# Kernel tuning notes

Measured on AMD Instinct MI355X. Metric: run time of the kernel, lower is better.

Reference implementation:

```python
import jax, jax.numpy as jnp
import numpy as np
from functools import partial

FACTOR = 5
N_HEADS = 16


def setup_inputs() -> dict:
    key = jax.random.key(0)
    ks = jax.random.split(key, 8)
    B, L, D = 4, 4096, 1024
    scale = 0.02
    return {
        "q": jax.random.normal(ks[0], (B, L, D), jnp.float32),
        "k": jax.random.normal(ks[1], (B, L, D), jnp.float32),
        "v": jax.random.normal(ks[2], (B, L, D), jnp.float32),
        "Wq": jax.random.normal(ks[3], (D, D), jnp.float32) * scale,
        "bq": jnp.zeros((D,), jnp.float32),
        "Wk": jax.random.normal(ks[4], (D, D), jnp.float32) * scale,
        "bk": jnp.zeros((D,), jnp.float32),
        "Wv": jax.random.normal(ks[5], (D, D), jnp.float32) * scale,
        "bv": jnp.zeros((D,), jnp.float32),
        "Wo": jax.random.normal(ks[6], (D, D), jnp.float32) * scale,
        "bo": jnp.zeros((D,), jnp.float32),
    }


def _time_delay_agg(values, corr):
    # values, corr: (B, H, L, C).  Faithful to the repo: the double mean
    # over dim=1 reduces head then LENGTH, leaving (B, C); top-k indices
    # therefore live in [0, C) and are reused as time delays.
    B, H, L, C = values.shape
    top_k = int(FACTOR * np.log(L + 1)) if L > 1 else 1
    top_k = max(1, min(top_k, L))
    mean_value = corr.mean(axis=1).mean(axis=1)          # (B, C)
    mean_across_batch = mean_value.mean(axis=0)          # (C,)
    actual_k = min(top_k, C)
    _, indices = jax.lax.top_k(mean_across_batch, actual_k)  # (k,)
    selected = mean_value[:, indices]                    # (B, k)
    weights = jax.nn.softmax(selected, axis=-1)          # (B, k)
    t = jnp.arange(L)

    def body(acc, inp):
        d, w = inp                                       # scalar delay, (B,) weight
        idx = (t + d) % L                                # circular shift == roll of doubled tensor
        acc = acc + values[:, :, idx, :] * w[:, None, None, None]
        return acc, None

    agg, _ = jax.lax.scan(body, jnp.zeros_like(values), (indices, weights.T))
    return agg


def reference(q, k, v, Wq, bq, Wk, bk, Wv, bv, Wo, bo):
    B, L, D = q.shape
    H = N_HEADS
    dk = D // H

    def proj(x, W, b):
        y = x @ W.T + b
        return y.reshape(B, L, H, dk).transpose(0, 2, 1, 3)  # (B,H,L,dk)

    Q = proj(q, Wq, bq).astype(jnp.float32)
    K = proj(k, Wk, bk).astype(jnp.float32)
    V = proj(v, Wv, bv).astype(jnp.float32)

    Qf = jnp.fft.rfft(Q, axis=2)
    Kf = jnp.fft.rfft(K, axis=2)
    R = jnp.fft.irfft(Qf * jnp.conj(Kf), n=L, axis=2)    # (B,H,L,dk) autocorrelation

    V_agg = _time_delay_agg(V, R)                        # (B,H,L,dk)
    V_agg = V_agg.transpose(0, 2, 1, 3).reshape(B, L, D)
    return V_agg @ Wo.T + bo
```

## Files before the change

### kernel.cpp

```cpp
#include <hip/hip_runtime.h>
#include <hip/hip_bf16.h>

#define Bn 4
#define Ln 4096
#define Dn 1024
#define Hn 16
#define KSEL 41
#define NT8 16

typedef __attribute__((ext_vector_type(8))) _Float16 f16x8;
typedef __attribute__((ext_vector_type(4))) float f32x4;

__device__ __forceinline__ unsigned short f2h(float f) {
    union { _Float16 h; unsigned short u; } c;
    c.h = (_Float16)f;
    return c.u;
}

__device__ __forceinline__ void gl2lds16(const unsigned short* g, unsigned short* l) {
    __builtin_amdgcn_global_load_lds(
        (const __attribute__((address_space(1))) unsigned int*)(uintptr_t)g,
        (__attribute__((address_space(3))) unsigned int*)(uintptr_t)l,
        16, 0, 0);
}
__device__ __forceinline__ void gl2lds16f(const float* g, float* l) {
    __builtin_amdgcn_global_load_lds(
        (const __attribute__((address_space(1))) unsigned int*)(uintptr_t)g,
        (__attribute__((address_space(3))) unsigned int*)(uintptr_t)l,
        16, 0, 0);
}

__global__ __launch_bounds__(256) void colsum_part(const float* __restrict__ q,
                                                   const float* __restrict__ k,
                                                   float* __restrict__ part) {
    int tb = blockIdx.y; int tensor = tb >> 2, b = tb & 3;
    const f32x4* src = (const f32x4*)((tensor ? k : q) + (size_t)b * Ln * Dn) + threadIdx.x;
    int t0 = blockIdx.x * 64;
    f32x4 a0 = (f32x4){0.f, 0.f, 0.f, 0.f};
    f32x4 a1 = (f32x4){0.f, 0.f, 0.f, 0.f};
    #pragma unroll 1
    for (int g = 0; g < 8; ++g) {
        const f32x4* p = src + (size_t)(t0 + g * 8) * 256;
        f32x4 v0 = __builtin_nontemporal_load(p + 0 * 256);
        f32x4 v1 = __builtin_nontemporal_load(p + 1 * 256);
        f32x4 v2 = __builtin_nontemporal_load(p + 2 * 256);
        f32x4 v3 = __builtin_nontemporal_load(p + 3 * 256);
        f32x4 v4 = __builtin_nontemporal_load(p + 4 * 256);
        f32x4 v5 = __builtin_nontemporal_load(p + 5 * 256);
        f32x4 v6 = __builtin_nontemporal_load(p + 6 * 256);
        f32x4 v7 = __builtin_nontemporal_load(p + 7 * 256);
        a0 += v0 + v2 + v4 + v6;
        a1 += v1 + v3 + v5 + v7;
    }
    f32x4 o = a0 + a1;
    ((f32x4*)part)[((size_t)tb * 64 + blockIdx.x) * 256 + threadIdx.x] = o;
}

__global__ void colsum_fin(const float* __restrict__ part, float* __restrict__ sums) {
    int tb = blockIdx.y; int d = blockIdx.x * 256 + threadIdx.x;
    float s = 0.f;
    for (int i = 0; i < 64; ++i) s += part[((size_t)tb * 64 + i) * 1024 + d];
    sums[(size_t)tb * 1024 + d] = s;
}

__global__ void proj_sums(const float* __restrict__ sums,
                          const float* __restrict__ Wq, const float* __restrict__ bq,
                          const float* __restrict__ Wk, const float* __restrict__ bk,
                          float* __restrict__ SQK) {
    int t = blockIdx.y;
    const float* W    = t ? Wk : Wq;
    const float* bias = t ? bk : bq;
    const float* sv   = sums + (size_t)t * 4 * 1024;
    __shared__ float s_sv[4 * 1024];
    for (int i = threadIdx.x; i < 4 * 1024; i += 256) s_sv[i] = sv[i];
    __syncthreads();
    int wave = threadIdx.x >> 6, lane = threadIdx.x & 63;
    for (int rr = 0; rr < 4; ++rr) {
        int j = blockIdx.x * 16 + rr * 4 + wave;
        float p[4] = {0.f, 0.f, 0.f, 0.f};
        for (int c = 0; c < 4; ++c) {
            float4 wv = *(const float4*)(W + (size_t)j * 1024 + c * 256 + lane * 4);
            #pragma unroll
            for (int b = 0; b < 4; ++b) {
                float4 s = *(const float4*)(s_sv + b * 1024 + c * 256 + lane * 4);
                p[b] += wv.x * s.x + wv.y * s.y + wv.z * s.z + wv.w * s.w;
            }
        }
        #pragma unroll
        for (int b = 0; b < 4; ++b)
            for (int off = 1; off < 64; off <<= 1) p[b] += __shfl_xor(p[b], off);
        if (lane == 0) {
            float bb = bias[j] * (float)Ln;
            #pragma unroll
            for (int b = 0; b < 4; ++b) SQK[((size_t)t * 4 + b) * 1024 + j] = p[b] + bb;
        }
    }
}

__global__ void stats_topk(const float* __restrict__ SQK, int* __restrict__ dly,
                           float* __restrict__ gp) {
    __shared__ float s_mv[4][64];
    __shared__ float mab[64];
    __shared__ float selv[4][KSEL];
    __shared__ int   s_dly[KSEL];
    int tid = threadIdx.x; int b = tid >> 6, c = tid & 63;
    const float* SQ = SQK; const float* SK = SQK + 4 * 1024;
    float s = 0.f;
    for (int h = 0; h < Hn; ++h)
        s += SQ[(size_t)b * 1024 + h * 64 + c] * SK[(size_t)b * 1024 + h * 64 + c];
    s_mv[b][c] = s * (1.0f / ((float)Hn * (float)Ln));
    __syncthreads();
    if (tid < 64) mab[c] = (s_mv[0][c] + s_mv[1][c] + s_mv[2][c] + s_mv[3][c]) * 0.25f;
    __syncthreads();
    if (tid < 64) {
        float my = mab[c];
        int rank = 0;
        for (int j = 0; j < 64; ++j) {
            float vj = mab[j];
            rank += (vj > my) || (vj == my && j < c);
        }
        if (rank < KSEL) {
            s_dly[rank] = c;
            dly[rank] = c;
            selv[0][rank] = s_mv[0][c]; selv[1][rank] = s_mv[1][c];
            selv[2][rank] = s_mv[2][c]; selv[3][rank] = s_mv[3][c];
        }
    }
    __syncthreads();
    if (tid < 256) gp[tid] = 0.f;
    __syncthreads();
    if (tid < 4) {
        float mx = -1e30f;
        for (int i = 0; i < KSEL; ++i) mx = fmaxf(mx, selv[tid][i]);
        float ss = 0.f;
        for (int i = 0; i < KSEL; ++i) ss += expf(selv[tid][i] - mx);
        float inv = 1.0f / ss;
        for (int i = 0; i < KSEL; ++i)
            gp[tid * 64 + s_dly[i]] = expf(selv[tid][i] - mx) * inv;
    }
}

__global__ void prep_w(const float* __restrict__ Wo, const float* __restrict__ Wv,
                       unsigned short* __restrict__ Wof, unsigned short* __restrict__ WvTf) {
    int bx = blockIdx.x * 32, by = blockIdx.y * 32;
    int x = threadIdx.x, y0 = threadIdx.y;
    if (blockIdx.z == 0) {
        for (int i = 0; i < 32; i += 8) {
            size_t idx = (size_t)(by + y0 + i) * 1024 + bx + x;
            Wof[idx] = f2h(Wo[idx]);
        }
    } else {
        __shared__ float t[32][33];
        for (int i = 0; i < 32; i += 8)
            t[y0 + i][x] = Wv[(size_t)(by + y0 + i) * 1024 + bx + x];
        __syncthreads();
        for (int i = 0; i < 32; i += 8)
            WvTf[(size_t)(bx + y0 + i) * 1024 + by + x] = f2h(t[x][y0 + i]);
    }
}

__global__ void bcvec_k(const float* __restrict__ Wo, const float* __restrict__ bv,
                        const float* __restrict__ bo, float* __restrict__ bc) {
    __shared__ float s_bv[1024];
    for (int i = threadIdx.x; i < 1024; i += 256) s_bv[i] = bv[i];
    __syncthreads();
    int wave = threadIdx.x >> 6, lane = threadIdx.x & 63;
    for (int rr = 0; rr < 4; ++rr) {
        int n = blockIdx.x * 16 + rr * 4 + wave;
        float p = 0.f;
        for (int c = 0; c < 4; ++c) {
            float4 wv = *(const float4*)(Wo + (size_t)n * 1024 + c * 256 + lane * 4);
            float4 s  = *(const float4*)(s_bv + c * 256 + lane * 4);
            p += wv.x * s.x + wv.y * s.y + wv.z * s.z + wv.w * s.w;
        }
        for (int off = 1; off < 64; off <<= 1) p += __shfl_xor(p, off);
        if (lane == 0) bc[n] = p + bo[n];
    }
}

#define FT 128
#define FC 64
#define FW 64
__global__ __launch_bounds__(256) void gather_fir(const float* __restrict__ v,
                                                  const float* __restrict__ gp,
                                                  unsigned short* __restrict__ Vf) {
    __shared__ float S[(FT + FW) * FC];
    int b = blockIdx.z, c0 = blockIdx.y * FC, t0 = blockIdx.x * FT;
    const float* Vb = v + (size_t)b * Ln * Dn;
    #pragma unroll
    for (int it = 0; it < 12; ++it) {
        int idx = it * 256 + threadIdx.x;
        int r = idx >> 4, cc = idx & 15;
        int gr = (t0 + r) & (Ln - 1);
        gl2lds16f(Vb + (size_t)gr * Dn + c0 + cc * 4, S + idx * 4);
    }
    __syncthreads();
    int c4 = threadIdx.x & 15, rg = threadIdx.x >> 4;
    const int base = rg * 8;
    float4 acc[8];
    #pragma unroll
    for (int i = 0; i < 8; ++i) acc[i] = make_float4(0.f, 0.f, 0.f, 0.f);
    #pragma unroll
    for (int tc = 0; tc < 2; ++tc) {
        float gc[32];
        #pragma unroll
        for (int j = 0; j < 8; ++j) {
            float4 gv = ((const float4*)(gp + b * 64 + tc * 32))[j];
            gc[j * 4 + 0] = gv.x; gc[j * 4 + 1] = gv.y;
            gc[j * 4 + 2] = gv.z; gc[j * 4 + 3] = gv.w;
        }
        #pragma unroll
        for (int w = 0; w < 39; ++w) {
            float4 x = *(const float4*)&S[(base + tc * 32 + w) * FC + c4 * 4];
            #pragma unroll
            for (int i = 0; i < 8; ++i) {
                int j = w - i;
                if (j >= 0 && j < 32) {
                    float wt = gc[j];
                    acc[i].x += wt * x.x; acc[i].y += wt * x.y;
                    acc[i].z += wt * x.z; acc[i].w += wt * x.w;
                }
            }
        }
    }
    #pragma unroll
    for (int i = 0; i < 8; ++i) {
        size_t idx = ((size_t)b * Ln + t0 + base + i) * Dn + c0 + c4 * 4;
        ushort4 o;
        o.x = f2h(acc[i].x); o.y = f2h(acc[i].y);
        o.z = f2h(acc[i].z); o.w = f2h(acc[i].w);
        *(ushort4*)&Vf[idx] = o;
    }
}

template <int BM, bool OUT_F16>
__global__ __launch_bounds__(256, 2) void gemm_f16(
    const unsigned short* __restrict__ A, const unsigned short* __restrict__ Bt,
    float* __restrict__ C, unsigned short* __restrict__ Cf,
    const float* __restrict__ bias,
    int N, int K, int nbx) {
    constexpr int FM = BM / 32;
    __shared__ unsigned short sA[BM * 32];
    __shared__ unsigned short sB[BM * 32];

    int nwg = gridDim.x;
    int bid = blockIdx.x;
    int swz = (bid % 8) * (nwg / 8) + bid / 8;
    int by = swz / nbx, bx = swz % nbx;

    const int wave = threadIdx.x >> 6, lane = threadIdx.x & 63;
    const int lrow = lane & 15, lk = (lane >> 4) * 8;
    const int wr = wave >> 1, wc = wave & 1;

    f32x4 acc[FM][FM];
    #pragma unroll
    for (int i = 0; i < FM; ++i)
        #pragma unroll
        for (int j = 0; j < FM; ++j) acc[i][j] = (f32x4){0.f, 0.f, 0.f, 0.f};

    const int srow = lane >> 2;
    const int skq  = (lane & 3) * 8;

    for (int k0 = 0; k0 < K; k0 += 32) {
        #pragma unroll
        for (int j = 0; j < BM / 64; ++j) {
            int chunk = j * 4 + wave;
            int row = chunk * 16 + srow;
            gl2lds16(A  + (size_t)((by * BM) + row) * K + k0 + skq, sA + chunk * 512);
            gl2lds16(Bt + (size_t)((bx * BM) + row) * K + k0 + skq, sB + chunk * 512);
        }
        __syncthreads();
        f16x8 bfrag[FM];
        #pragma unroll
        for (int j = 0; j < FM; ++j) {
            int r = wc * (BM / 2) + j * 16 + lrow;
            bfrag[j] = *(const f16x8*)&sB[r * 32 + lk];
        }
        #pragma unroll
        for (int i = 0; i < FM; ++i) {
            int r = wr * (BM / 2) + i * 16 + lrow;
            f16x8 afrag = *(const f16x8*)&sA[r * 32 + lk];
            #pragma unroll
            for (int j = 0; j < FM; ++j)
                acc[i][j] = __builtin_amdgcn_mfma_f32_16x16x32_f16(afrag, bfrag[j], acc[i][j], 0, 0, 0);
        }
        __syncthreads();
    }
    #pragma unroll
    for (int i = 0; i < FM; ++i) {
        int r0 = by * BM + wr * (BM / 2) + i * 16 + (lane >> 4) * 4;
        #pragma unroll
        for (int j = 0; j < FM; ++j) {
            int c = bx * BM + wc * (BM / 2) + j * 16 + (lane & 15);
            float bb = OUT_F16 ? 0.f : bias[c];
            #pragma unroll
            for (int r = 0; r < 4; ++r) {
                size_t idx = (size_t)(r0 + r) * N + c;
                if (OUT_F16) Cf[idx] = f2h(acc[i][j][r]);
                else         C[idx]  = acc[i][j][r] + bb;
            }
        }
    }
}

__device__ __forceinline__ void mm16q(const f16x8* a, const f16x8* b, f32x4 (&acc)[2][4]) {
    #pragma unroll
    for (int i = 0; i < 2; ++i)
        #pragma unroll
        for (int j = 0; j < 4; ++j)
            #pragma unroll
            for (int s = 0; s < 2; ++s)
                acc[i][j] = __builtin_amdgcn_mfma_f32_16x16x32_f16(a[i * 2 + s], b[j * 2 + s],
                                                                   acc[i][j], 0, 0, 0);
}

__global__ __launch_bounds__(512, 2) void gemm8p(const unsigned short* __restrict__ A,
                                                 const unsigned short* __restrict__ Bt,
                                                 float* __restrict__ C,
                                                 const float* __restrict__ bias) {
    __shared__ unsigned short lds[65536];
    int bid = blockIdx.x;
    int swz = (bid & 7) * 32 + (bid >> 3);
    int by = swz >> 2, bx = swz & 3;

    const int tid = threadIdx.x;
    const int wv = tid >> 6, lane = tid & 63;
    const int wr = wv >> 1, wc = wv & 1;
    const int srow = lane >> 3, sslot = lane & 7;

    f32x4 acc[4][2][4];
    #pragma unroll
    for (int q = 0; q < 4; ++q)
        #pragma unroll
        for (int i = 0; i < 2; ++i)
            #pragma unroll
            for (int j = 0; j < 4; ++j) acc[q][i][j] = (f32x4){0.f, 0.f, 0.f, 0.f};

    auto STAGE = [&](int t, int op, int mh) {
        unsigned short* hb = lds + ((((t & 1) * 2 + op) * 2 + mh) << 13);
        const unsigned short* G = op ? Bt : A;
        int base_row = (op ? bx : by) * 256 + mh * 128;
        #pragma unroll
        for (int i = 0; i < 2; ++i) {
            int rl = i * 64 + wv * 8 + srow;
            int cs = sslot ^ (rl & 7);
            gl2lds16(G + (size_t)(base_row + rl) * 1024 + t * 64 + cs * 8,
                     hb + i * 4096 + wv * 512);
        }
    };
    auto LDA = [&](int t, int h, f16x8* a) {
        const unsigned short* hb = lds + ((((t & 1) * 2 + 0) * 2 + h) << 13);
        #pragma unroll
        for (int i = 0; i < 2; ++i) {
            int rl = wr * 32 + i * 16 + (lane & 15);
            #pragma unroll
            for (int s = 0; s < 2; ++s) {
                int cs = s * 4 + (lane >> 4);
                a[i * 2 + s] = *(const f16x8*)(hb + rl * 64 + ((cs ^ (rl & 7)) << 3));
            }
        }
    };
    auto LDB = [&](int t, int h, f16x8* b) {
        const unsigned short* hb = lds + ((((t & 1) * 2 + 1) * 2 + h) << 13);
        #pragma unroll
        for (int j = 0; j < 4; ++j) {
            int rl = wc * 64 + j * 16 + (lane & 15);
            #pragma unroll
            for (int s = 0; s < 2; ++s) {
                int cs = s * 4 + (lane >> 4);
                b[j * 2 + s] = *(const f16x8*)(hb + rl * 64 + ((cs ^ (rl & 7)) << 3));
            }
        }
    };

    STAGE(0, 0, 0); STAGE(0, 1, 0); STAGE(0, 0, 1); STAGE(0, 1, 1);
    STAGE(1, 0, 0); STAGE(1, 1, 0); STAGE(1, 0, 1);
    asm volatile("s_waitcnt vmcnt(6)" ::: "memory");
    __builtin_amdgcn_s_barrier();

    f16x8 a0[4], a1[4], b[8];
    for (int t = 0; t < NT8; ++t) {
        const bool p1 = (t + 1 < NT8), p2 = (t + 2 < NT8);
        LDA(t, 0, a0); LDB(t, 0, b);
        if (p1) STAGE(t + 1, 1, 1);
        __builtin_amdgcn_s_barrier();
        asm volatile("s_waitcnt lgkmcnt(0)" ::: "memory");
        __builtin_amdgcn_sched_barrier(0);
        __builtin_amdgcn_s_setprio(1);
        mm16q(a0, b, acc[0]);
        __builtin_amdgcn_s_setprio(0);
        __builtin_amdgcn_s_barrier();
        LDA(t, 1, a1);
        if (p2) STAGE(t + 2, 0, 0);
        __builtin_amdgcn_s_barrier();
        asm volatile("s_waitcnt lgkmcnt(0)" ::: "memory");
        __builtin_amdgcn_sched_barrier(0);
        __builtin_amdgcn_s_setprio(1);
        mm16q(a1, b, acc[2]);
        __builtin_amdgcn_s_setprio(0);
        __builtin_amdgcn_s_barrier();
        LDB(t, 1, b);
        if (p2) STAGE(t + 2, 1, 0);
        __builtin_amdgcn_s_barrier();
        asm volatile("s_waitcnt lgkmcnt(0)" ::: "memory");
        __builtin_amdgcn_sched_barrier(0);
        __builtin_amdgcn_s_setprio(1);
        mm16q(a0, b, acc[1]);
        __builtin_amdgcn_s_setprio(0);
        __builtin_amdgcn_s_barrier();
        if (p2) STAGE(t + 2, 0, 1);
        if (p2) { asm volatile("s_waitcnt vmcnt(6)" ::: "memory"); }
        else    { asm volatile("s_waitcnt vmcnt(0)" ::: "memory"); }
        __builtin_amdgcn_s_barrier();
        __builtin_amdgcn_s_setprio(1);
        mm16q(a1, b, acc[3]);
        __builtin_amdgcn_s_setprio(0);
        __builtin_amdgcn_s_barrier();
    }

    const int lr = (lane >> 4) << 2, lc = lane & 15;
    #pragma unroll
    for (int q = 0; q < 4; ++q) {
        int rbase = by * 256 + (q >> 1) * 128 + wr * 32 + lr;
        int cbase = bx * 256 + (q & 1) * 128 + wc * 64 + lc;
        #pragma unroll
        for (int j = 0; j < 4; ++j) {
            int c = cbase + j * 16;
            float bb = bias[c];
            #pragma unroll
            for (int i = 0; i < 2; ++i)
                #pragma unroll
                for (int r = 0; r < 4; ++r)
                    C[(size_t)(rbase + i * 16 + r) * 1024 + c] = acc[q][i][j][r] + bb;
        }
    }
}

extern "C" void kernel_launch(void* const* d_in, const int* in_sizes, int n_in,
                              void* d_out, int out_size, void* d_ws, size_t ws_size,
                              hipStream_t stream) {
    const float* q  = (const float*)d_in[0];
    const float* k  = (const float*)d_in[1];
    const float* v  = (const float*)d_in[2];
    const float* Wq = (const float*)d_in[3];
    const float* bq = (const float*)d_in[4];
    const float* Wk = (const float*)d_in[5];
    const float* bk = (const float*)d_in[6];
    const float* Wv = (const float*)d_in[7];
    const float* bv = (const float*)d_in[8];
    const float* Wo = (const float*)d_in[9];
    const float* bo = (const float*)d_in[10];
    float* out = (float*)d_out;
    float* ws  = (float*)d_ws;

    unsigned short* Vf    = (unsigned short*)ws;
    unsigned short* Wof   = Vf + 16777216;
    unsigned short* WvTf  = Wof + 1048576;
    unsigned short* Wcf   = WvTf + 1048576;
    float* part = (float*)(Wcf + 1048576);
    float* sums = part + 524288;
    float* SQK  = sums + 8192;
    float* gp   = SQK + 8192;
    float* bc   = gp + 256;
    int*   dly  = (int*)(bc + 1024);

    hipLaunchKernelGGL(colsum_part, dim3(64, 8), dim3(256), 0, stream, q, k, part);
    hipLaunchKernelGGL(colsum_fin, dim3(4, 8), dim3(256), 0, stream, part, sums);
    hipLaunchKernelGGL(proj_sums, dim3(64, 2), dim3(256), 0, stream, sums, Wq, bq, Wk, bk, SQK);
    hipLaunchKernelGGL(stats_topk, dim3(1), dim3(256), 0, stream, SQK, dly, gp);

    hipLaunchKernelGGL(prep_w, dim3(32, 32, 2), dim3(32, 8), 0, stream, Wo, Wv, Wof, WvTf);
    hipLaunchKernelGGL((gemm_f16<64, true>), dim3(256), dim3(256), 0, stream,
                       Wof, WvTf, (float*)nullptr, Wcf, (const float*)nullptr,
                       1024, 1024, 16);
    hipLaunchKernelGGL(bcvec_k, dim3(64), dim3(256), 0, stream, Wo, bv, bo, bc);

    hipLaunchKernelGGL(gather_fir, dim3(32, 16, 4), dim3(256), 0, stream, v, gp, Vf);

    hipLaunchKernelGGL(gemm8p, dim3(256), dim3(512), 0, stream, Vf, Wcf, out, bc);
}
```

Baseline: 135.3 us.

## Merge column sums, weight combine GEMM and bias vector into one prework kernel

Replaces four launches (colsum_part, prep_w, gemm_f16, bcvec_k) with a single heterogeneous kernel whose block ranges do the column sums, a Wo·Wv fp16 MFMA GEMM that converts and transposes fp32 in-register into LDS, and the bias vector. This removes launch gaps and the intermediate fp16 weight copies, and lets the small weight work overlap with the bandwidth-bound column sums. The fused GEMM loses the async global-to-LDS loads and stores the transposed B tile with scalar 2-byte LDS writes, which may bank-conflict. The final GEMM output also switches to nontemporal stores.

```diff
diff --git a/kernel.cpp b/kernel.cpp
--- a/kernel.cpp
+++ b/kernel.cpp
@@ -30,30 +30,120 @@
         16, 0, 0);
 }
 
-__global__ __launch_bounds__(256) void colsum_part(const float* __restrict__ q,
-                                                   const float* __restrict__ k,
-                                                   float* __restrict__ part) {
-    int tb = blockIdx.y; int tensor = tb >> 2, b = tb & 3;
-    const f32x4* src = (const f32x4*)((tensor ? k : q) + (size_t)b * Ln * Dn) + threadIdx.x;
-    int t0 = blockIdx.x * 64;
-    f32x4 a0 = (f32x4){0.f, 0.f, 0.f, 0.f};
-    f32x4 a1 = (f32x4){0.f, 0.f, 0.f, 0.f};
-    #pragma unroll 1
-    for (int g = 0; g < 8; ++g) {
-        const f32x4* p = src + (size_t)(t0 + g * 8) * 256;
-        f32x4 v0 = __builtin_nontemporal_load(p + 0 * 256);
-        f32x4 v1 = __builtin_nontemporal_load(p + 1 * 256);
-        f32x4 v2 = __builtin_nontemporal_load(p + 2 * 256);
-        f32x4 v3 = __builtin_nontemporal_load(p + 3 * 256);
-        f32x4 v4 = __builtin_nontemporal_load(p + 4 * 256);
-        f32x4 v5 = __builtin_nontemporal_load(p + 5 * 256);
-        f32x4 v6 = __builtin_nontemporal_load(p + 6 * 256);
-        f32x4 v7 = __builtin_nontemporal_load(p + 7 * 256);
-        a0 += v0 + v2 + v4 + v6;
-        a1 += v1 + v3 + v5 + v7;
-    }
-    f32x4 o = a0 + a1;
-    ((f32x4*)part)[((size_t)tb * 64 + blockIdx.x) * 256 + threadIdx.x] = o;
+__global__ __launch_bounds__(256) void prework(const float* __restrict__ q,
+                                               const float* __restrict__ k,
+                                               const float* __restrict__ Wq_unused,
+                                               const float* __restrict__ Wo,
+                                               const float* __restrict__ Wv,
+                                               const float* __restrict__ bv,
+                                               const float* __restrict__ bo,
+                                               float* __restrict__ part,
+                                               unsigned short* __restrict__ Wcf,
+                                               float* __restrict__ bc) {
+    __shared__ __align__(16) unsigned short sAB[2][64 * 32];
+    int bid = blockIdx.x;
+    int tid = threadIdx.x;
+
+    if (bid < 512) {
+        int cx = bid & 63, tb = bid >> 6;
+        int tensor = tb >> 2, b = tb & 3;
+        const f32x4* src = (const f32x4*)((tensor ? k : q) + (size_t)b * Ln * Dn) + tid;
+        int t0 = cx * 64;
+        f32x4 a0 = (f32x4){0.f, 0.f, 0.f, 0.f};
+        f32x4 a1 = (f32x4){0.f, 0.f, 0.f, 0.f};
+        #pragma unroll 1
+        for (int g = 0; g < 8; ++g) {
+            const f32x4* p = src + (size_t)(t0 + g * 8) * 256;
+            f32x4 v0 = __builtin_nontemporal_load(p + 0 * 256);
+            f32x4 v1 = __builtin_nontemporal_load(p + 1 * 256);
+            f32x4 v2 = __builtin_nontemporal_load(p + 2 * 256);
+            f32x4 v3 = __builtin_nontemporal_load(p + 3 * 256);
+            f32x4 v4 = __builtin_nontemporal_load(p + 4 * 256);
+            f32x4 v5 = __builtin_nontemporal_load(p + 5 * 256);
+            f32x4 v6 = __builtin_nontemporal_load(p + 6 * 256);
+            f32x4 v7 = __builtin_nontemporal_load(p + 7 * 256);
+            a0 += v0 + v2 + v4 + v6;
+            a1 += v1 + v3 + v5 + v7;
+        }
+        f32x4 o = a0 + a1;
+        ((f32x4*)part)[((size_t)tb * 64 + cx) * 256 + tid] = o;
+    } else if (bid < 768) {
+        unsigned short* sA = sAB[0];
+        unsigned short* sB = sAB[1];
+        int b2 = bid - 512;
+        int n0 = (b2 >> 4) * 64, k0 = (b2 & 15) * 64;
+        const int wv = tid >> 6, lane = tid & 63;
+        const int wr = wv >> 1, wc = wv & 1;
+        const int lrow = lane & 15, lk = (lane >> 4) * 8;
+        f32x4 acc[2][2];
+        #pragma unroll
+        for (int i = 0; i < 2; ++i)
+            #pragma unroll
+            for (int j = 0; j < 2; ++j) acc[i][j] = (f32x4){0.f, 0.f, 0.f, 0.f};
+        for (int j0 = 0; j0 < 1024; j0 += 32) {
+            #pragma unroll
+            for (int s = 0; s < 2; ++s) {
+                int id = tid + s * 256;
+                int ar = id >> 3, ac = (id & 7) * 4;
+                float4 av = *(const float4*)&Wo[(size_t)(n0 + ar) * 1024 + j0 + ac];
+                ushort4 ah;
+                ah.x = f2h(av.x); ah.y = f2h(av.y); ah.z = f2h(av.z); ah.w = f2h(av.w);
+                *(ushort4*)&sA[ar * 32 + ac] = ah;
+                int jr = id >> 4, kc = (id & 15) * 4;
+                float4 bvv = *(const float4*)&Wv[(size_t)(j0 + jr) * 1024 + k0 + kc];
+                sB[(kc + 0) * 32 + jr] = f2h(bvv.x);
+                sB[(kc + 1) * 32 + jr] = f2h(bvv.y);
+                sB[(kc + 2) * 32 + jr] = f2h(bvv.z);
+                sB[(kc + 3) * 32 + jr] = f2h(bvv.w);
+            }
+            __syncthreads();
+            f16x8 af[2], bf[2];
+            #pragma unroll
+            for (int i = 0; i < 2; ++i) {
+                int r = wr * 32 + i * 16 + lrow;
+                af[i] = *(const f16x8*)&sA[r * 32 + lk];
+            }
+            #pragma unroll
+            for (int j = 0; j < 2; ++j) {
+                int c = wc * 32 + j * 16 + lrow;
+                bf[j] = *(const f16x8*)&sB[c * 32 + lk];
+            }
+            #pragma unroll
+            for (int i = 0; i < 2; ++i)
+                #pragma unroll
+                for (int j = 0; j < 2; ++j)
+                    acc[i][j] = __builtin_amdgcn_mfma_f32_16x16x32_f16(af[i], bf[j], acc[i][j], 0, 0, 0);
+            __syncthreads();
+        }
+        #pragma unroll
+        for (int i = 0; i < 2; ++i) {
+            int r0 = n0 + wr * 32 + i * 16 + (lane >> 4) * 4;
+            #pragma unroll
+            for (int j = 0; j < 2; ++j) {
+                int c = k0 + wc * 32 + j * 16 + (lane & 15);
+                #pragma unroll
+                for (int r = 0; r < 4; ++r)
+                    Wcf[(size_t)(r0 + r) * 1024 + c] = f2h(acc[i][j][r]);
+            }
+        }
+    } else {
+        float* s_bv = (float*)sAB;
+        int b3 = bid - 768;
+        for (int i = tid; i < 1024; i += 256) s_bv[i] = bv[i];
+        __syncthreads();
+        int wv = tid >> 6, lane = tid & 63;
+        for (int rr = 0; rr < 4; ++rr) {
+            int n = b3 * 16 + rr * 4 + wv;
+            float p = 0.f;
+            for (int c = 0; c < 4; ++c) {
+                float4 w4 = *(const float4*)(Wo + (size_t)n * 1024 + c * 256 + lane * 4);
+                float4 s4 = *(const float4*)(s_bv + c * 256 + lane * 4);
+                p += w4.x * s4.x + w4.y * s4.y + w4.z * s4.z + w4.w * s4.w;
+            }
+            for (int off = 1; off < 64; off <<= 1) p += __shfl_xor(p, off);
+            if (lane == 0) bc[n] = p + bo[n];
+        }
+    }
 }
 
 __global__ void colsum_fin(const float* __restrict__ part, float* __restrict__ sums) {
@@ -140,44 +230,6 @@
     }
 }
 
-__global__ void prep_w(const float* __restrict__ Wo, const float* __restrict__ Wv,
-                       unsigned short* __restrict__ Wof, unsigned short* __restrict__ WvTf) {
-    int bx = blockIdx.x * 32, by = blockIdx.y * 32;
-    int x = threadIdx.x, y0 = threadIdx.y;
-    if (blockIdx.z == 0) {
-        for (int i = 0; i < 32; i += 8) {
-            size_t idx = (size_t)(by + y0 + i) * 1024 + bx + x;
-            Wof[idx] = f2h(Wo[idx]);
-        }
-    } else {
-        __shared__ float t[32][33];
-        for (int i = 0; i < 32; i += 8)
-            t[y0 + i][x] = Wv[(size_t)(by + y0 + i) * 1024 + bx + x];
-        __syncthreads();
-        for (int i = 0; i < 32; i += 8)
-            WvTf[(size_t)(bx + y0 + i) * 1024 + by + x] = f2h(t[x][y0 + i]);
-    }
-}
-
-__global__ void bcvec_k(const float* __restrict__ Wo, const float* __restrict__ bv,
-                        const float* __restrict__ bo, float* __restrict__ bc) {
-    __shared__ float s_bv[1024];
-    for (int i = threadIdx.x; i < 1024; i += 256) s_bv[i] = bv[i];
-    __syncthreads();
-    int wave = threadIdx.x >> 6, lane = threadIdx.x & 63;
-    for (int rr = 0; rr < 4; ++rr) {
-        int n = blockIdx.x * 16 + rr * 4 + wave;
-        float p = 0.f;
-        for (int c = 0; c < 4; ++c) {
-            float4 wv = *(const float4*)(Wo + (size_t)n * 1024 + c * 256 + lane * 4);
-            float4 s  = *(const float4*)(s_bv + c * 256 + lane * 4);
-            p += wv.x * s.x + wv.y * s.y + wv.z * s.z + wv.w * s.w;
-        }
-        for (int off = 1; off < 64; off <<= 1) p += __shfl_xor(p, off);
-        if (lane == 0) bc[n] = p + bo[n];
-    }
-}
-
 #define FT 128
 #define FC 64
 #define FW 64
@@ -233,76 +285,6 @@
     }
 }
 
-template <int BM, bool OUT_F16>
-__global__ __launch_bounds__(256, 2) void gemm_f16(
-    const unsigned short* __restrict__ A, const unsigned short* __restrict__ Bt,
-    float* __restrict__ C, unsigned short* __restrict__ Cf,
-    const float* __restrict__ bias,
-    int N, int K, int nbx) {
-    constexpr int FM = BM / 32;
-    __shared__ unsigned short sA[BM * 32];
-    __shared__ unsigned short sB[BM * 32];
-
-    int nwg = gridDim.x;
-    int bid = blockIdx.x;
-    int swz = (bid % 8) * (nwg / 8) + bid / 8;
-    int by = swz / nbx, bx = swz % nbx;
-
-    const int wave = threadIdx.x >> 6, lane = threadIdx.x & 63;
-    const int lrow = lane & 15, lk = (lane >> 4) * 8;
-    const int wr = wave >> 1, wc = wave & 1;
-
-    f32x4 acc[FM][FM];
-    #pragma unroll
-    for (int i = 0; i < FM; ++i)
-        #pragma unroll
-        for (int j = 0; j < FM; ++j) acc[i][j] = (f32x4){0.f, 0.f, 0.f, 0.f};
-
-    const int srow = lane >> 2;
-    const int skq  = (lane & 3) * 8;
-
-    for (int k0 = 0; k0 < K; k0 += 32) {
-        #pragma unroll
-        for (int j = 0; j < BM / 64; ++j) {
-            int chunk = j * 4 + wave;
-            int row = chunk * 16 + srow;
-            gl2lds16(A  + (size_t)((by * BM) + row) * K + k0 + skq, sA + chunk * 512);
-            gl2lds16(Bt + (size_t)((bx * BM) + row) * K + k0 + skq, sB + chunk * 512);
-        }
-        __syncthreads();
-        f16x8 bfrag[FM];
-        #pragma unroll
-        for (int j = 0; j < FM; ++j) {
-            int r = wc * (BM / 2) + j * 16 + lrow;
-            bfrag[j] = *(const f16x8*)&sB[r * 32 + lk];
-        }
-        #pragma unroll
-        for (int i = 0; i < FM; ++i) {
-            int r = wr * (BM / 2) + i * 16 + lrow;
-            f16x8 afrag = *(const f16x8*)&sA[r * 32 + lk];
-            #pragma unroll
-            for (int j = 0; j < FM; ++j)
-                acc[i][j] = __builtin_amdgcn_mfma_f32_16x16x32_f16(afrag, bfrag[j], acc[i][j], 0, 0, 0);
-        }
-        __syncthreads();
-    }
-    #pragma unroll
-    for (int i = 0; i < FM; ++i) {
-        int r0 = by * BM + wr * (BM / 2) + i * 16 + (lane >> 4) * 4;
-        #pragma unroll
-        for (int j = 0; j < FM; ++j) {
-            int c = bx * BM + wc * (BM / 2) + j * 16 + (lane & 15);
-            float bb = OUT_F16 ? 0.f : bias[c];
-            #pragma unroll
-            for (int r = 0; r < 4; ++r) {
-                size_t idx = (size_t)(r0 + r) * N + c;
-                if (OUT_F16) Cf[idx] = f2h(acc[i][j][r]);
-                else         C[idx]  = acc[i][j][r] + bb;
-            }
-        }
-    }
-}
-
 __device__ __forceinline__ void mm16q(const f16x8* a, const f16x8* b, f32x4 (&acc)[2][4]) {
     #pragma unroll
     for (int i = 0; i < 2; ++i)
@@ -431,7 +413,8 @@
             for (int i = 0; i < 2; ++i)
                 #pragma unroll
                 for (int r = 0; r < 4; ++r)
-                    C[(size_t)(rbase + i * 16 + r) * 1024 + c] = acc[q][i][j][r] + bb;
+                    __builtin_nontemporal_store(acc[q][i][j][r] + bb,
+                                                &C[(size_t)(rbase + i * 16 + r) * 1024 + c]);
         }
     }
 }
@@ -453,10 +436,8 @@
     float* out = (float*)d_out;
     float* ws  = (float*)d_ws;
 
-    unsigned short* Vf    = (unsigned short*)ws;
-    unsigned short* Wof   = Vf + 16777216;
-    unsigned short* WvTf  = Wof + 1048576;
-    unsigned short* Wcf   = WvTf + 1048576;
+    unsigned short* Vf  = (unsigned short*)ws;
+    unsigned short* Wcf = Vf + 16777216;
     float* part = (float*)(Wcf + 1048576);
     float* sums = part + 524288;
     float* SQK  = sums + 8192;
@@ -464,17 +445,13 @@
     float* bc   = gp + 256;
     int*   dly  = (int*)(bc + 1024);
 
-    hipLaunchKernelGGL(colsum_part, dim3(64, 8), dim3(256), 0, stream, q, k, part);
+    hipLaunchKernelGGL(prework, dim3(832), dim3(256), 0, stream,
+                       q, k, Wq, Wo, Wv, bv, bo, part, Wcf, bc);
+
     hipLaunchKernelGGL(colsum_fin, dim3(4, 8), dim3(256), 0, stream, part, sums);
     hipLaunchKernelGGL(proj_sums, dim3(64, 2), dim3(256), 0, stream, sums, Wq, bq, Wk, bk, SQK);
     hipLaunchKernelGGL(stats_topk, dim3(1), dim3(256), 0, stream, SQK, dly, gp);
 
-    hipLaunchKernelGGL(prep_w, dim3(32, 32, 2), dim3(32, 8), 0, stream, Wo, Wv, Wof, WvTf);
-    hipLaunchKernelGGL((gemm_f16<64, true>), dim3(256), dim3(256), 0, stream,
-                       Wof, WvTf, (float*)nullptr, Wcf, (const float*)nullptr,
-                       1024, 1024, 16);
-    hipLaunchKernelGGL(bcvec_k, dim3(64), dim3(256), 0, stream, Wo, bv, bo, bc);
-
     hipLaunchKernelGGL(gather_fir, dim3(32, 16, 4), dim3(256), 0, stream, v, gp, Vf);
 
     hipLaunchKernelGGL(gemm8p, dim3(256), dim3(512), 0, stream, Vf, Wcf, out, bc);
```

Result: slower. 141.2 us (+4.4%).
